# Performance work log

Hardware: AMD Instinct MI355X
Metric: run time of the kernel (lower is better)

The kernel has to match this reference:

```python
import jax, jax.numpy as jnp
import numpy as np
from jax import lax

D_MODEL = 1024
D_FF = 4096
K = 5
PAD = K // 2


def setup_inputs() -> dict:
    key = jax.random.key(0)
    ks = jax.random.split(key, 12)
    s_in = 1.0 / np.sqrt(D_MODEL)
    s_ff = 1.0 / np.sqrt(D_FF)
    s_k = 1.0 / np.sqrt(K)  # depthwise conv fan_in = 1*K
    return {
        "x": jax.random.normal(ks[0], (4, 2048, D_MODEL), dtype=jnp.float32),
        "Wg": jax.random.uniform(ks[1], (D_MODEL, D_FF), jnp.float32, -s_in, s_in),
        "bg": jax.random.uniform(ks[2], (D_FF,), jnp.float32, -s_in, s_in),
        "Wu": jax.random.uniform(ks[3], (D_MODEL, D_FF), jnp.float32, -s_in, s_in),
        "bu": jax.random.uniform(ks[4], (D_FF,), jnp.float32, -s_in, s_in),
        "convg_w": jax.random.uniform(ks[5], (D_FF, 1, K), jnp.float32, -s_k, s_k),
        "convg_b": jax.random.uniform(ks[6], (D_FF,), jnp.float32, -s_k, s_k),
        "convu_w": jax.random.uniform(ks[7], (D_FF, 1, K), jnp.float32, -s_k, s_k),
        "convu_b": jax.random.uniform(ks[8], (D_FF,), jnp.float32, -s_k, s_k),
        "Wd": jax.random.uniform(ks[9], (D_FF, D_MODEL), jnp.float32, -s_ff, s_ff),
        "bd": jax.random.uniform(ks[10], (D_MODEL,), jnp.float32, -s_ff, s_ff),
    }


def _dwconv(h, w, b):
    # h: [B, L, C] -> depthwise conv along L with 'same' padding -> [B, L, C]
    y = lax.conv_general_dilated(
        h.transpose(0, 2, 1),  # [B, C, L]
        w,                      # [C, 1, K]
        window_strides=(1,),
        padding=[(PAD, PAD)],
        feature_group_count=h.shape[-1],
    )
    return (y + b[None, :, None]).transpose(0, 2, 1)


def reference(x, Wg, bg, Wu, bu, convg_w, convg_b, convu_w, convu_b, Wd, bd):
    gate = _dwconv(jnp.einsum("bld,df->blf", x, Wg) + bg, convg_w, convg_b)
    up = _dwconv(jnp.einsum("bld,df->blf", x, Wu) + bu, convu_w, convu_b)
    h = jax.nn.silu(gate) * up
    return jnp.einsum("blf,fd->bld", h, Wd) + bd
```

## Files before the change

### kernel.cpp

```cpp
#include <hip/hip_runtime.h>
#include <hip/hip_bf16.h>
#include <cstdint>

#define BATCH  4
#define SEQ    2048
#define DMODEL 1024
#define DFF    4096
#define MTOT   (BATCH * SEQ)
#define KCONV  5
#define PADC   2

using bf16raw = unsigned short;
typedef __attribute__((ext_vector_type(8))) short bf16x8;
typedef __attribute__((ext_vector_type(4))) float f32x4;

__device__ __forceinline__ float bf2f(bf16raw u) {
    return __uint_as_float(((uint32_t)u) << 16);
}
__device__ __forceinline__ bf16raw f2bf(float f) {
    uint32_t u = __float_as_uint(f);
    u = (u + 0x7fffu + ((u >> 16) & 1u)) >> 16;
    return (bf16raw)u;
}


__global__ __launch_bounds__(256)
void cvt_bf16_kernel(const float* __restrict__ in, bf16raw* __restrict__ out, int n4)
{
    const int i = blockIdx.x * 256 + threadIdx.x;
    if (i >= n4) return;
    const float4 v = reinterpret_cast<const float4*>(in)[i];
    ushort4 o;
    o.x = f2bf(v.x); o.y = f2bf(v.y); o.z = f2bf(v.z); o.w = f2bf(v.w);
    reinterpret_cast<ushort4*>(out)[i] = o;
}

__global__ __launch_bounds__(256)
void transpose_cvt_kernel(const float* __restrict__ in, bf16raw* __restrict__ out,
                          int R, int C)
{
    __shared__ float tile[32][33];
    const int r0 = blockIdx.y * 32, c0 = blockIdx.x * 32;
    const int tx = threadIdx.x & 31, ty = threadIdx.x >> 5;
#pragma unroll
    for (int i = 0; i < 4; ++i)
        tile[ty + i * 8][tx] = in[(size_t)(r0 + ty + i * 8) * C + c0 + tx];
    __syncthreads();
#pragma unroll
    for (int i = 0; i < 4; ++i)
        out[(size_t)(c0 + ty + i * 8) * R + r0 + tx] = f2bf(tile[tx][ty + i * 8]);
}

__global__ __launch_bounds__(256)
void convw_reorder_kernel(const float* __restrict__ wg, const float* __restrict__ wu,
                          float* __restrict__ wgT, float* __restrict__ wuT)
{
    const int i = blockIdx.x * 256 + threadIdx.x;
    if (i >= KCONV * DFF) return;
    const int j = i / DFF, f = i - j * DFF;
    wgT[i] = wg[f * KCONV + j];
    wuT[i] = wu[f * KCONV + j];
}


__device__ __forceinline__ void async_load16(const bf16raw* g, bf16raw* lds)
{
    __builtin_amdgcn_global_load_lds(
        (const __attribute__((address_space(1))) void*)g,
        (__attribute__((address_space(3))) void*)lds, 16, 0, 0);
}

template<typename CT>
__global__ __launch_bounds__(256)
void mfma_gemm_kernel(const bf16raw* __restrict__ A, const bf16raw* __restrict__ BT,
                      const float* __restrict__ bias, CT* __restrict__ C,
                      int N, int K)
{
    __shared__ __align__(16) bf16raw smem[2 * 128 * 64];
    bf16raw* As = smem;
    bf16raw* Bs = smem + 128 * 64;

    const int tid  = threadIdx.x;
    const int lane = tid & 63;
    const int wave = __builtin_amdgcn_readfirstlane(tid >> 6);
    const int bm = blockIdx.y * 128;
    const int bn = blockIdx.x * 128;
    const int wm = (wave >> 1) * 64;
    const int wn = (wave & 1) * 64;

    const int srow = (wave << 3) + (lane >> 3);
    const int scol = (lane & 7) << 3;
    const bf16raw* Ag = A  + (size_t)(bm + srow) * K + scol;
    const bf16raw* Bg = BT + (size_t)(bn + srow) * K + scol;

    f32x4 acc[4][4];
#pragma unroll
    for (int i = 0; i < 4; ++i)
#pragma unroll
        for (int j = 0; j < 4; ++j) acc[i][j] = (f32x4){0.f, 0.f, 0.f, 0.f};

    for (int k0 = 0; k0 < K; k0 += 64) {
        __syncthreads();
#pragma unroll
        for (int r = 0; r < 4; ++r) {
            async_load16(Ag + (size_t)(r * 32) * K + k0, As + r * 2048 + wave * 512);
            async_load16(Bg + (size_t)(r * 32) * K + k0, Bs + r * 2048 + wave * 512);
        }
        asm volatile("s_waitcnt vmcnt(0)" ::: "memory");
        __syncthreads();

#pragma unroll
        for (int kk = 0; kk < 2; ++kk) {
            const int kb = kk * 32 + ((lane >> 4) << 3);
            bf16x8 a[4], b[4];
#pragma unroll
            for (int i = 0; i < 4; ++i) {
                a[i] = *reinterpret_cast<const bf16x8*>(As + (wm + i * 16 + (lane & 15)) * 64 + kb);
                b[i] = *reinterpret_cast<const bf16x8*>(Bs + (wn + i * 16 + (lane & 15)) * 64 + kb);
            }
#pragma unroll
            for (int mi = 0; mi < 4; ++mi)
#pragma unroll
                for (int ni = 0; ni < 4; ++ni)
                    acc[mi][ni] = __builtin_amdgcn_mfma_f32_16x16x32_bf16(
                        a[mi], b[ni], acc[mi][ni], 0, 0, 0);
        }
    }

    const int crow0 = (lane >> 4) << 2;
    const int ccol  = lane & 15;
#pragma unroll
    for (int ni = 0; ni < 4; ++ni) {
        const int n = bn + wn + ni * 16 + ccol;
        const float bs = bias[n];
#pragma unroll
        for (int mi = 0; mi < 4; ++mi) {
            const int mbase = bm + wm + mi * 16 + crow0;
#pragma unroll
            for (int j = 0; j < 4; ++j) {
                const float v = acc[mi][ni][j] + bs;
                if constexpr (sizeof(CT) == 2)
                    C[(size_t)(mbase + j) * N + n] = f2bf(v);
                else
                    C[(size_t)(mbase + j) * N + n] = v;
            }
        }
    }
}

__global__ __launch_bounds__(256)
void conv_silu_mul_bf16_kernel(const bf16raw* __restrict__ gp, const bf16raw* __restrict__ up,
                               const float* __restrict__ wgT, const float* __restrict__ cbg,
                               const float* __restrict__ wuT, const float* __restrict__ cbu,
                               bf16raw* __restrict__ h, int rows)
{
    const int idx = blockIdx.x * 256 + threadIdx.x;
    const int f   = (idx & (DFF / 8 - 1)) << 3;
    const int row = idx >> 9;
    if (row >= rows) return;
    const int l = row & (SEQ - 1);

    float g[8], u[8];
    {
        const float4 a0 = *reinterpret_cast<const float4*>(cbg + f);
        const float4 a1 = *reinterpret_cast<const float4*>(cbg + f + 4);
        const float4 b0 = *reinterpret_cast<const float4*>(cbu + f);
        const float4 b1 = *reinterpret_cast<const float4*>(cbu + f + 4);
        g[0]=a0.x; g[1]=a0.y; g[2]=a0.z; g[3]=a0.w; g[4]=a1.x; g[5]=a1.y; g[6]=a1.z; g[7]=a1.w;
        u[0]=b0.x; u[1]=b0.y; u[2]=b0.z; u[3]=b0.w; u[4]=b1.x; u[5]=b1.y; u[6]=b1.z; u[7]=b1.w;
    }

#pragma unroll
    for (int j = 0; j < KCONV; ++j) {
        const int ls = l + j - PADC;
        if (ls < 0 || ls >= SEQ) continue;
        const size_t off = (size_t)(row + j - PADC) * DFF + f;
        const bf16x8 gv = *reinterpret_cast<const bf16x8*>(gp + off);
        const bf16x8 uv = *reinterpret_cast<const bf16x8*>(up + off);
        const float4 wa0 = *reinterpret_cast<const float4*>(wgT + j * DFF + f);
        const float4 wa1 = *reinterpret_cast<const float4*>(wgT + j * DFF + f + 4);
        const float4 wb0 = *reinterpret_cast<const float4*>(wuT + j * DFF + f);
        const float4 wb1 = *reinterpret_cast<const float4*>(wuT + j * DFF + f + 4);
        const float wg8[8] = {wa0.x, wa0.y, wa0.z, wa0.w, wa1.x, wa1.y, wa1.z, wa1.w};
        const float wu8[8] = {wb0.x, wb0.y, wb0.z, wb0.w, wb1.x, wb1.y, wb1.z, wb1.w};
#pragma unroll
        for (int c = 0; c < 8; ++c) {
            g[c] += bf2f((bf16raw)gv[c]) * wg8[c];
            u[c] += bf2f((bf16raw)uv[c]) * wu8[c];
        }
    }

    bf16x8 hv;
#pragma unroll
    for (int c = 0; c < 8; ++c) {
        const float s = g[c] / (1.f + __expf(-g[c]));
        hv[c] = (short)f2bf(s * u[c]);
    }
    *reinterpret_cast<bf16x8*>(h + (size_t)row * DFF + f) = hv;
}


#define BM 128
#define BN 128
#define BK 8

__device__ __forceinline__ void load4(const float* p, float v[4]) {
    const float4 t = *reinterpret_cast<const float4*>(p);
    v[0] = t.x; v[1] = t.y; v[2] = t.z; v[3] = t.w;
}
__device__ __forceinline__ void load4(const bf16raw* p, float v[4]) {
    const ushort4 t = *reinterpret_cast<const ushort4*>(p);
    v[0] = bf2f(t.x); v[1] = bf2f(t.y); v[2] = bf2f(t.z); v[3] = bf2f(t.w);
}
__device__ __forceinline__ void store4(float* p, const float v[4]) {
    float4 t; t.x = v[0]; t.y = v[1]; t.z = v[2]; t.w = v[3];
    *reinterpret_cast<float4*>(p) = t;
}
__device__ __forceinline__ void store4(bf16raw* p, const float v[4]) {
    ushort4 t; t.x = f2bf(v[0]); t.y = f2bf(v[1]); t.z = f2bf(v[2]); t.w = f2bf(v[3]);
    *reinterpret_cast<ushort4*>(p) = t;
}

template<typename AT, typename CT>
__global__ __launch_bounds__(256)
void sgemm_bias_kernel(const AT* __restrict__ A, const float* __restrict__ B,
                       const float* __restrict__ bias, CT* __restrict__ C,
                       int N, int K)
{
    __shared__ float As[BK][BM];
    __shared__ float Bs[BK][BN];

    const int tid = threadIdx.x;
    const int bm  = blockIdx.y * BM;
    const int bn  = blockIdx.x * BN;
    const int tx  = tid & 15;
    const int ty  = tid >> 4;

    const int arow = tid >> 1;
    const int acol = (tid & 1) * 4;
    const int brow = tid >> 5;
    const int bcol = (tid & 31) * 4;

    const AT*    Ap = A + (size_t)(bm + arow) * K + acol;
    const float* Bp = B + (size_t)brow * N + bn + bcol;

    float acc[8][8];
#pragma unroll
    for (int i = 0; i < 8; ++i)
#pragma unroll
        for (int j = 0; j < 8; ++j) acc[i][j] = 0.f;

    for (int k0 = 0; k0 < K; k0 += BK) {
        float av[4];
        load4(Ap + k0, av);
        const float4 bv = *reinterpret_cast<const float4*>(Bp + (size_t)k0 * N);

        __syncthreads();
#pragma unroll
        for (int i = 0; i < 4; ++i) As[acol + i][arow] = av[i];
        *reinterpret_cast<float4*>(&Bs[brow][bcol]) = bv;
        __syncthreads();

#pragma unroll
        for (int kk = 0; kk < BK; ++kk) {
            const float4 a0 = *reinterpret_cast<const float4*>(&As[kk][ty * 4]);
            const float4 a1 = *reinterpret_cast<const float4*>(&As[kk][64 + ty * 4]);
            const float4 b0 = *reinterpret_cast<const float4*>(&Bs[kk][tx * 4]);
            const float4 b1 = *reinterpret_cast<const float4*>(&Bs[kk][64 + tx * 4]);
            const float am[8] = {a0.x, a0.y, a0.z, a0.w, a1.x, a1.y, a1.z, a1.w};
            const float bb[8] = {b0.x, b0.y, b0.z, b0.w, b1.x, b1.y, b1.z, b1.w};
#pragma unroll
            for (int mi = 0; mi < 8; ++mi)
#pragma unroll
                for (int nj = 0; nj < 8; ++nj)
                    acc[mi][nj] += am[mi] * bb[nj];
        }
    }

#pragma unroll
    for (int mi = 0; mi < 8; ++mi) {
        const int m = bm + ((mi < 4) ? (ty * 4 + mi) : (64 + ty * 4 + (mi - 4)));
#pragma unroll
        for (int g = 0; g < 2; ++g) {
            const int n = bn + g * 64 + tx * 4;
            float o[4];
#pragma unroll
            for (int c = 0; c < 4; ++c) o[c] = acc[mi][g * 4 + c] + bias[n + c];
            store4(&C[(size_t)m * N + n], o);
        }
    }
}

template<typename PT, typename HT>
__global__ __launch_bounds__(256)
void conv_silu_mul_kernel(const PT* __restrict__ gp, const PT* __restrict__ up,
                          const float* __restrict__ wg, const float* __restrict__ cbg,
                          const float* __restrict__ wu, const float* __restrict__ cbu,
                          HT* __restrict__ hout)
{
    const int idx = blockIdx.x * 256 + threadIdx.x;
    const int f   = (idx & (DFF / 4 - 1)) * 4;
    const int l   = idx >> 10;

    float g[4], u[4];
    load4(cbg + f, g);
    load4(cbu + f, u);

#pragma unroll
    for (int j = 0; j < KCONV; ++j) {
        const int ls = l + j - PADC;
        if (ls < 0 || ls >= SEQ) continue;
        const size_t off = (size_t)ls * DFF + f;
        float gv[4], uv[4];
        load4(gp + off, gv);
        load4(up + off, uv);
#pragma unroll
        for (int c = 0; c < 4; ++c) {
            g[c] += gv[c] * wg[(f + c) * KCONV + j];
            u[c] += uv[c] * wu[(f + c) * KCONV + j];
        }
    }

    float h[4];
#pragma unroll
    for (int c = 0; c < 4; ++c) {
        const float s = g[c] / (1.f + __expf(-g[c]));
        h[c] = s * u[c];
    }
    store4(hout + (size_t)l * DFF + f, h);
}


extern "C" void kernel_launch(void* const* d_in, const int* in_sizes, int n_in,
                              void* d_out, int out_size, void* d_ws, size_t ws_size,
                              hipStream_t stream)
{
    const float* x   = (const float*)d_in[0];
    const float* Wg  = (const float*)d_in[1];
    const float* bg  = (const float*)d_in[2];
    const float* Wu  = (const float*)d_in[3];
    const float* bu  = (const float*)d_in[4];
    const float* cgw = (const float*)d_in[5];
    const float* cgb = (const float*)d_in[6];
    const float* cuw = (const float*)d_in[7];
    const float* cub = (const float*)d_in[8];
    const float* Wd  = (const float*)d_in[9];
    const float* bd  = (const float*)d_in[10];
    float* out = (float*)d_out;

    const dim3 blk(256);

    const size_t SZ_XB  = (size_t)MTOT * DMODEL * 2;
    const size_t SZ_W   = (size_t)DFF * DMODEL * 2;
    const size_t SZ_CW  = (size_t)KCONV * DFF * 4;
    const size_t SZ_PF  = (size_t)MTOT * DFF * 2;
    const size_t SZ_PB  = (size_t)SEQ  * DFF * 2;

    auto align256 = [](size_t v) { return (v + 255) & ~(size_t)255; };

    size_t cur = 0;
    const size_t oXB  = cur; cur = align256(cur + SZ_XB);
    const size_t oWgT = cur; cur = align256(cur + SZ_W);
    const size_t oWuT = cur; cur = align256(cur + SZ_W);
    const size_t oWdT = cur; cur = align256(cur + SZ_W);
    const size_t oCWg = cur; cur = align256(cur + SZ_CW);
    const size_t oCWu = cur; cur = align256(cur + SZ_CW);
    const size_t oH   = cur; cur = align256(cur + SZ_PF);
    const size_t oPRE = cur;
    const size_t needT1 = oPRE + 2 * align256(SZ_PF);
    const size_t needT2 = oPRE + 2 * align256(SZ_PB);

    if (ws_size >= needT2) {
        bf16raw* xb  = (bf16raw*)((char*)d_ws + oXB);
        bf16raw* WgT = (bf16raw*)((char*)d_ws + oWgT);
        bf16raw* WuT = (bf16raw*)((char*)d_ws + oWuT);
        bf16raw* WdT = (bf16raw*)((char*)d_ws + oWdT);
        float*   cwg = (float*)((char*)d_ws + oCWg);
        float*   cwu = (float*)((char*)d_ws + oCWu);
        bf16raw* h   = (bf16raw*)((char*)d_ws + oH);

        cvt_bf16_kernel<<<(MTOT * DMODEL / 4 + 255) / 256, blk, 0, stream>>>(x, xb, MTOT * DMODEL / 4);
        transpose_cvt_kernel<<<dim3(DFF / 32, DMODEL / 32), blk, 0, stream>>>(Wg, WgT, DMODEL, DFF);
        transpose_cvt_kernel<<<dim3(DFF / 32, DMODEL / 32), blk, 0, stream>>>(Wu, WuT, DMODEL, DFF);
        transpose_cvt_kernel<<<dim3(DMODEL / 32, DFF / 32), blk, 0, stream>>>(Wd, WdT, DFF, DMODEL);
        convw_reorder_kernel<<<(KCONV * DFF + 255) / 256, blk, 0, stream>>>(cgw, cuw, cwg, cwu);

        if (ws_size >= needT1) {
            bf16raw* gpre = (bf16raw*)((char*)d_ws + oPRE);
            bf16raw* upre = (bf16raw*)((char*)d_ws + oPRE + align256(SZ_PF));
            dim3 gu(DFF / 128, MTOT / 128);
            mfma_gemm_kernel<bf16raw><<<gu, blk, 0, stream>>>(xb, WgT, bg, gpre, DFF, DMODEL);
            mfma_gemm_kernel<bf16raw><<<gu, blk, 0, stream>>>(xb, WuT, bu, upre, DFF, DMODEL);
            const int nconv = MTOT * (DFF / 8) / 256;
            conv_silu_mul_bf16_kernel<<<nconv, blk, 0, stream>>>(gpre, upre, cwg, cgb, cwu, cub, h, MTOT);
        } else {
            bf16raw* gpre = (bf16raw*)((char*)d_ws + oPRE);
            bf16raw* upre = (bf16raw*)((char*)d_ws + oPRE + align256(SZ_PB));
            dim3 gu(DFF / 128, SEQ / 128);
            const int nconv = SEQ * (DFF / 8) / 256;
            for (int b = 0; b < BATCH; ++b) {
                const bf16raw* xbb = xb + (size_t)b * SEQ * DMODEL;
                mfma_gemm_kernel<bf16raw><<<gu, blk, 0, stream>>>(xbb, WgT, bg, gpre, DFF, DMODEL);
                mfma_gemm_kernel<bf16raw><<<gu, blk, 0, stream>>>(xbb, WuT, bu, upre, DFF, DMODEL);
                conv_silu_mul_bf16_kernel<<<nconv, blk, 0, stream>>>(
                    gpre, upre, cwg, cgb, cwu, cub, h + (size_t)b * SEQ * DFF, SEQ);
            }
        }
        dim3 gd(DMODEL / 128, MTOT / 128);
        mfma_gemm_kernel<float><<<gd, blk, 0, stream>>>(h, WdT, bd, out, DMODEL, DFF);
        return;
    }

    const size_t CE  = (size_t)SEQ * DFF;
    const size_t P32 = CE * sizeof(float);
    const size_t P16 = CE * sizeof(bf16raw);

    dim3 gu(DFF / BN, SEQ / BM);
    dim3 gdc(DMODEL / BN, SEQ / BM);
    const int nconv = SEQ * (DFF / 4) / 256;

    if (ws_size >= 3 * P32) {
        float* gpre = (float*)d_ws;
        float* upre = gpre + CE;
        float* hbuf = upre + CE;
        for (int b = 0; b < BATCH; ++b) {
            const float* xbp = x + (size_t)b * SEQ * DMODEL;
            float* outb = out + (size_t)b * SEQ * DMODEL;
            sgemm_bias_kernel<float, float><<<gu, blk, 0, stream>>>(xbp, Wg, bg, gpre, DFF, DMODEL);
            sgemm_bias_kernel<float, float><<<gu, blk, 0, stream>>>(xbp, Wu, bu, upre, DFF, DMODEL);
            conv_silu_mul_kernel<float, float><<<nconv * 2, blk, 0, stream>>>(
                gpre, upre, cgw, cgb, cuw, cub, hbuf);
            sgemm_bias_kernel<float, float><<<gdc, blk, 0, stream>>>(hbuf, Wd, bd, outb, DMODEL, DFF);
        }
    } else if (ws_size >= 3 * P16) {
        bf16raw* gpre = (bf16raw*)d_ws;
        bf16raw* upre = gpre + CE;
        bf16raw* hbuf = upre + CE;
        for (int b = 0; b < BATCH; ++b) {
            const float* xbp = x + (size_t)b * SEQ * DMODEL;
            float* outb = out + (size_t)b * SEQ * DMODEL;
            sgemm_bias_kernel<float, bf16raw><<<gu, blk, 0, stream>>>(xbp, Wg, bg, gpre, DFF, DMODEL);
            sgemm_bias_kernel<float, bf16raw><<<gu, blk, 0, stream>>>(xbp, Wu, bu, upre, DFF, DMODEL);
            conv_silu_mul_kernel<bf16raw, bf16raw><<<nconv * 2, blk, 0, stream>>>(
                gpre, upre, cgw, cgb, cuw, cub, hbuf);
            sgemm_bias_kernel<bf16raw, float><<<gdc, blk, 0, stream>>>(hbuf, Wd, bd, outb, DMODEL, DFF);
        }
    }
}
```

Measured before the change: 441.5 us.

## Use 256x256 double-buffered MFMA GEMM with fused gate/up and split-K down projection

Result: faster. 386.2 us (-12.5%).

```diff
diff --git a/kernel.cpp b/kernel.cpp
--- a/kernel.cpp
+++ b/kernel.cpp
@@ -63,102 +63,165 @@
 }
 
 
-__device__ __forceinline__ void async_load16(const bf16raw* g, bf16raw* lds)
+__device__ __forceinline__ void gll16(const bf16raw* g, const char* lds)
 {
     __builtin_amdgcn_global_load_lds(
         (const __attribute__((address_space(1))) void*)g,
         (__attribute__((address_space(3))) void*)lds, 16, 0, 0);
 }
 
-template<typename CT>
-__global__ __launch_bounds__(256)
-void mfma_gemm_kernel(const bf16raw* __restrict__ A, const bf16raw* __restrict__ BT,
-                      const float* __restrict__ bias, CT* __restrict__ C,
-                      int N, int K)
-{
-    __shared__ __align__(16) bf16raw smem[2 * 128 * 64];
-    bf16raw* As = smem;
-    bf16raw* Bs = smem + 128 * 64;
+template<typename CT, bool BIAS, int SPLITK>
+__global__ __launch_bounds__(512, 2)
+void gemm256_kernel(const bf16raw* __restrict__ A, const bf16raw* __restrict__ BT,
+                    const float* __restrict__ bias0, const float* __restrict__ bias1,
+                    CT* __restrict__ C, int M, int N, int K, int nbm, int nbn)
+{
+    __shared__ __align__(16) char smem[131072];
 
     const int tid  = threadIdx.x;
     const int lane = tid & 63;
     const int wave = __builtin_amdgcn_readfirstlane(tid >> 6);
-    const int bm = blockIdx.y * 128;
-    const int bn = blockIdx.x * 128;
-    const int wm = (wave >> 1) * 64;
-    const int wn = (wave & 1) * 64;
-
-    const int srow = (wave << 3) + (lane >> 3);
-    const int scol = (lane & 7) << 3;
-    const bf16raw* Ag = A  + (size_t)(bm + srow) * K + scol;
-    const bf16raw* Bg = BT + (size_t)(bn + srow) * K + scol;
-
-    f32x4 acc[4][4];
-#pragma unroll
-    for (int i = 0; i < 4; ++i)
+    const int wr = wave >> 2;
+    const int wc = wave & 3;
+
+    const int nwg = nbm * nbn * SPLITK;
+    const int cpx = nwg >> 3;
+    const int bid = blockIdx.x;
+    const int swz = (bid & 7) * cpx + (bid >> 3);
+    int sk = 0, rem = swz;
+    if constexpr (SPLITK > 1) { sk = swz / (nbm * nbn); rem = swz - sk * (nbm * nbn); }
+    const int bx = rem / nbm;
+    const int by = rem - bx * nbm;
+    const int bm = by * 256;
+    const int bn = bx * 256;
+
+    const int klen = K / SPLITK;
+    const int kbeg = sk * klen;
+    const int NT   = klen / 64;
+    CT* Cp = C + (size_t)sk * M * N;
+
+    const int srow = tid >> 3;
+    const int kswz = (((tid & 7) ^ ((tid >> 3) & 7)) << 3);
+    const bf16raw* Asrc = A  + (size_t)(bm + srow) * K + kbeg + kswz;
+    const bf16raw* Bsrc = BT + (size_t)(bn + srow) * K + kbeg + kswz;
+
+    const int g4  = lane >> 4;
+    const int r15 = lane & 15;
+    const int key = lane & 7;
+    const int off0 = r15 * 128 + (((0 + g4) ^ key) << 4);
+    const int off1 = r15 * 128 + (((4 + g4) ^ key) << 4);
+
+    f32x4 acc[8][4];
+#pragma unroll
+    for (int i = 0; i < 8; ++i)
 #pragma unroll
         for (int j = 0; j < 4; ++j) acc[i][j] = (f32x4){0.f, 0.f, 0.f, 0.f};
 
-    for (int k0 = 0; k0 < K; k0 += 64) {
-        __syncthreads();
-#pragma unroll
-        for (int r = 0; r < 4; ++r) {
-            async_load16(Ag + (size_t)(r * 32) * K + k0, As + r * 2048 + wave * 512);
-            async_load16(Bg + (size_t)(r * 32) * K + k0, Bs + r * 2048 + wave * 512);
-        }
-        asm volatile("s_waitcnt vmcnt(0)" ::: "memory");
-        __syncthreads();
-
-#pragma unroll
-        for (int kk = 0; kk < 2; ++kk) {
-            const int kb = kk * 32 + ((lane >> 4) << 3);
-            bf16x8 a[4], b[4];
-#pragma unroll
-            for (int i = 0; i < 4; ++i) {
-                a[i] = *reinterpret_cast<const bf16x8*>(As + (wm + i * 16 + (lane & 15)) * 64 + kb);
-                b[i] = *reinterpret_cast<const bf16x8*>(Bs + (wn + i * 16 + (lane & 15)) * 64 + kb);
+    auto stage = [&](int t, int buf) {
+        const bf16raw* Ag = Asrc + (size_t)t * 64;
+        const bf16raw* Bg = Bsrc + (size_t)t * 64;
+        const char* la = smem + buf * 65536 + tid * 16;
+        const char* lb = la + 32768;
+#pragma unroll
+        for (int i = 0; i < 4; ++i) {
+            gll16(Ag + (size_t)i * 64 * K, la + i * 8192);
+            gll16(Bg + (size_t)i * 64 * K, lb + i * 8192);
+        }
+    };
+
+    auto compute = [&](int buf) {
+        const char* bufA = smem + buf * 65536 + wr * 16384;
+        const char* bufB = smem + buf * 65536 + 32768 + wc * 8192;
+        bf16x8 bfr[4][2];
+#pragma unroll
+        for (int nf = 0; nf < 4; ++nf) {
+            bfr[nf][0] = *(const bf16x8*)(bufB + nf * 2048 + off0);
+            bfr[nf][1] = *(const bf16x8*)(bufB + nf * 2048 + off1);
+        }
+#pragma unroll
+        for (int q = 0; q < 4; ++q) {
+            bf16x8 afr[2][2];
+#pragma unroll
+            for (int m2 = 0; m2 < 2; ++m2) {
+                afr[m2][0] = *(const bf16x8*)(bufA + (q * 2 + m2) * 2048 + off0);
+                afr[m2][1] = *(const bf16x8*)(bufA + (q * 2 + m2) * 2048 + off1);
             }
-#pragma unroll
-            for (int mi = 0; mi < 4; ++mi)
-#pragma unroll
-                for (int ni = 0; ni < 4; ++ni)
-                    acc[mi][ni] = __builtin_amdgcn_mfma_f32_16x16x32_bf16(
-                        a[mi], b[ni], acc[mi][ni], 0, 0, 0);
-        }
-    }
-
-    const int crow0 = (lane >> 4) << 2;
-    const int ccol  = lane & 15;
-#pragma unroll
-    for (int ni = 0; ni < 4; ++ni) {
-        const int n = bn + wn + ni * 16 + ccol;
-        const float bs = bias[n];
-#pragma unroll
-        for (int mi = 0; mi < 4; ++mi) {
-            const int mbase = bm + wm + mi * 16 + crow0;
+            __builtin_amdgcn_s_setprio(1);
+#pragma unroll
+            for (int m2 = 0; m2 < 2; ++m2)
+#pragma unroll
+                for (int nf = 0; nf < 4; ++nf) {
+                    acc[q * 2 + m2][nf] = __builtin_amdgcn_mfma_f32_16x16x32_bf16(
+                        afr[m2][0], bfr[nf][0], acc[q * 2 + m2][nf], 0, 0, 0);
+                    acc[q * 2 + m2][nf] = __builtin_amdgcn_mfma_f32_16x16x32_bf16(
+                        afr[m2][1], bfr[nf][1], acc[q * 2 + m2][nf], 0, 0, 0);
+                }
+            __builtin_amdgcn_s_setprio(0);
+        }
+    };
+
+    stage(0, 0);
+    for (int t = 0; t < NT; ++t) {
+        const int cur = t & 1;
+        if (t + 1 < NT) {
+            stage(t + 1, cur ^ 1);
+            asm volatile("s_waitcnt vmcnt(8)" ::: "memory");
+        } else {
+            asm volatile("s_waitcnt vmcnt(0)" ::: "memory");
+        }
+        __builtin_amdgcn_s_barrier();
+        compute(cur);
+        __builtin_amdgcn_s_barrier();
+        asm volatile("" ::: "memory");
+    }
+
+    const int er = g4 << 2;
+#pragma unroll
+    for (int nf = 0; nf < 4; ++nf) {
+        const int nn = bn + wc * 64 + nf * 16 + r15;
+        float bv = 0.f;
+        if constexpr (BIAS) bv = (nn < DFF) ? bias0[nn] : bias1[nn - DFF];
+#pragma unroll
+        for (int mf = 0; mf < 8; ++mf) {
+            const int mrow = bm + wr * 128 + mf * 16 + er;
 #pragma unroll
             for (int j = 0; j < 4; ++j) {
-                const float v = acc[mi][ni][j] + bs;
+                const float v = acc[mf][nf][j] + bv;
                 if constexpr (sizeof(CT) == 2)
-                    C[(size_t)(mbase + j) * N + n] = f2bf(v);
+                    Cp[(size_t)(mrow + j) * N + nn] = f2bf(v);
                 else
-                    C[(size_t)(mbase + j) * N + n] = v;
+                    Cp[(size_t)(mrow + j) * N + nn] = v;
             }
         }
     }
+}
+
+__global__ __launch_bounds__(256)
+void reduce_bias_kernel(const float* __restrict__ part, const float* __restrict__ bd,
+                        float* __restrict__ out)
+{
+    const int i = blockIdx.x * 256 + threadIdx.x;
+    const int d = (i & (DMODEL / 4 - 1)) * 4;
+    const float4 a = reinterpret_cast<const float4*>(part)[i];
+    const float4 b = reinterpret_cast<const float4*>(part + (size_t)MTOT * DMODEL)[i];
+    const float4 bb = *reinterpret_cast<const float4*>(bd + d);
+    float4 o;
+    o.x = a.x + b.x + bb.x; o.y = a.y + b.y + bb.y;
+    o.z = a.z + b.z + bb.z; o.w = a.w + b.w + bb.w;
+    reinterpret_cast<float4*>(out)[i] = o;
 }
 
 __global__ __launch_bounds__(256)
 void conv_silu_mul_bf16_kernel(const bf16raw* __restrict__ gp, const bf16raw* __restrict__ up,
                                const float* __restrict__ wgT, const float* __restrict__ cbg,
                                const float* __restrict__ wuT, const float* __restrict__ cbu,
-                               bf16raw* __restrict__ h, int rows)
+                               bf16raw* __restrict__ h, int S)
 {
     const int idx = blockIdx.x * 256 + threadIdx.x;
     const int f   = (idx & (DFF / 8 - 1)) << 3;
     const int row = idx >> 9;
-    if (row >= rows) return;
-    const int l = row & (SEQ - 1);
+    const int l   = row & (SEQ - 1);
+    const int rb  = row - l;
 
     float g[8], u[8];
     {
@@ -174,7 +237,7 @@
     for (int j = 0; j < KCONV; ++j) {
         const int ls = l + j - PADC;
         if (ls < 0 || ls >= SEQ) continue;
-        const size_t off = (size_t)(row + j - PADC) * DFF + f;
+        const size_t off = (size_t)(rb + ls) * S + f;
         const bf16x8 gv = *reinterpret_cast<const bf16x8*>(gp + off);
         const bf16x8 uv = *reinterpret_cast<const bf16x8*>(up + off);
         const float4 wa0 = *reinterpret_cast<const float4*>(wgT + j * DFF + f);
@@ -204,27 +267,14 @@
 #define BN 128
 #define BK 8
 
-__device__ __forceinline__ void load4(const float* p, float v[4]) {
+__device__ __forceinline__ void load4f(const float* p, float v[4]) {
     const float4 t = *reinterpret_cast<const float4*>(p);
     v[0] = t.x; v[1] = t.y; v[2] = t.z; v[3] = t.w;
 }
-__device__ __forceinline__ void load4(const bf16raw* p, float v[4]) {
-    const ushort4 t = *reinterpret_cast<const ushort4*>(p);
-    v[0] = bf2f(t.x); v[1] = bf2f(t.y); v[2] = bf2f(t.z); v[3] = bf2f(t.w);
-}
-__device__ __forceinline__ void store4(float* p, const float v[4]) {
-    float4 t; t.x = v[0]; t.y = v[1]; t.z = v[2]; t.w = v[3];
-    *reinterpret_cast<float4*>(p) = t;
-}
-__device__ __forceinline__ void store4(bf16raw* p, const float v[4]) {
-    ushort4 t; t.x = f2bf(v[0]); t.y = f2bf(v[1]); t.z = f2bf(v[2]); t.w = f2bf(v[3]);
-    *reinterpret_cast<ushort4*>(p) = t;
-}
-
-template<typename AT, typename CT>
-__global__ __launch_bounds__(256)
-void sgemm_bias_kernel(const AT* __restrict__ A, const float* __restrict__ B,
-                       const float* __restrict__ bias, CT* __restrict__ C,
+
+__global__ __launch_bounds__(256)
+void sgemm_bias_kernel(const float* __restrict__ A, const float* __restrict__ B,
+                       const float* __restrict__ bias, float* __restrict__ C,
                        int N, int K)
 {
     __shared__ float As[BK][BM];
@@ -241,7 +291,7 @@
     const int brow = tid >> 5;
     const int bcol = (tid & 31) * 4;
 
-    const AT*    Ap = A + (size_t)(bm + arow) * K + acol;
+    const float* Ap = A + (size_t)(bm + arow) * K + acol;
     const float* Bp = B + (size_t)brow * N + bn + bcol;
 
     float acc[8][8];
@@ -252,15 +302,13 @@
 
     for (int k0 = 0; k0 < K; k0 += BK) {
         float av[4];
-        load4(Ap + k0, av);
+        load4f(Ap + k0, av);
         const float4 bv = *reinterpret_cast<const float4*>(Bp + (size_t)k0 * N);
-
         __syncthreads();
 #pragma unroll
         for (int i = 0; i < 4; ++i) As[acol + i][arow] = av[i];
         *reinterpret_cast<float4*>(&Bs[brow][bcol]) = bv;
         __syncthreads();
-
 #pragma unroll
         for (int kk = 0; kk < BK; ++kk) {
             const float4 a0 = *reinterpret_cast<const float4*>(&As[kk][ty * 4]);
@@ -276,58 +324,57 @@
                     acc[mi][nj] += am[mi] * bb[nj];
         }
     }
-
 #pragma unroll
     for (int mi = 0; mi < 8; ++mi) {
         const int m = bm + ((mi < 4) ? (ty * 4 + mi) : (64 + ty * 4 + (mi - 4)));
 #pragma unroll
         for (int g = 0; g < 2; ++g) {
             const int n = bn + g * 64 + tx * 4;
-            float o[4];
-#pragma unroll
-            for (int c = 0; c < 4; ++c) o[c] = acc[mi][g * 4 + c] + bias[n + c];
-            store4(&C[(size_t)m * N + n], o);
-        }
-    }
-}
-
-template<typename PT, typename HT>
-__global__ __launch_bounds__(256)
-void conv_silu_mul_kernel(const PT* __restrict__ gp, const PT* __restrict__ up,
-                          const float* __restrict__ wg, const float* __restrict__ cbg,
-                          const float* __restrict__ wu, const float* __restrict__ cbu,
-                          HT* __restrict__ hout)
+            float4 o;
+            o.x = acc[mi][g * 4 + 0] + bias[n + 0];
+            o.y = acc[mi][g * 4 + 1] + bias[n + 1];
+            o.z = acc[mi][g * 4 + 2] + bias[n + 2];
+            o.w = acc[mi][g * 4 + 3] + bias[n + 3];
+            *reinterpret_cast<float4*>(&C[(size_t)m * N + n]) = o;
+        }
+    }
+}
+
+__global__ __launch_bounds__(256)
+void conv_silu_mul_f32_kernel(const float* __restrict__ gp, const float* __restrict__ up,
+                              const float* __restrict__ wg, const float* __restrict__ cbg,
+                              const float* __restrict__ wu, const float* __restrict__ cbu,
+                              float* __restrict__ hout)
 {
     const int idx = blockIdx.x * 256 + threadIdx.x;
     const int f   = (idx & (DFF / 4 - 1)) * 4;
     const int l   = idx >> 10;
 
     float g[4], u[4];
-    load4(cbg + f, g);
-    load4(cbu + f, u);
-
+    load4f(cbg + f, g);
+    load4f(cbu + f, u);
 #pragma unroll
     for (int j = 0; j < KCONV; ++j) {
         const int ls = l + j - PADC;
         if (ls < 0 || ls >= SEQ) continue;
         const size_t off = (size_t)ls * DFF + f;
         float gv[4], uv[4];
-        load4(gp + off, gv);
-        load4(up + off, uv);
+        load4f(gp + off, gv);
+        load4f(up + off, uv);
 #pragma unroll
         for (int c = 0; c < 4; ++c) {
             g[c] += gv[c] * wg[(f + c) * KCONV + j];
             u[c] += uv[c] * wu[(f + c) * KCONV + j];
         }
     }
-
     float h[4];
 #pragma unroll
     for (int c = 0; c < 4; ++c) {
         const float s = g[c] / (1.f + __expf(-g[c]));
         h[c] = s * u[c];
     }
-    store4(hout + (size_t)l * DFF + f, h);
+    float4 o; o.x = h[0]; o.y = h[1]; o.z = h[2]; o.w = h[3];
+    *reinterpret_cast<float4*>(&hout[(size_t)l * DFF + f]) = o;
 }
 
 
@@ -349,101 +396,75 @@
     float* out = (float*)d_out;
 
     const dim3 blk(256);
+    auto align256 = [](size_t v) { return (v + 255) & ~(size_t)255; };
 
     const size_t SZ_XB  = (size_t)MTOT * DMODEL * 2;
-    const size_t SZ_W   = (size_t)DFF * DMODEL * 2;
+    const size_t SZ_WGU = (size_t)2 * DFF * DMODEL * 2;
+    const size_t SZ_WD  = (size_t)DMODEL * DFF * 2;
     const size_t SZ_CW  = (size_t)KCONV * DFF * 4;
-    const size_t SZ_PF  = (size_t)MTOT * DFF * 2;
-    const size_t SZ_PB  = (size_t)SEQ  * DFF * 2;
-
-    auto align256 = [](size_t v) { return (v + 255) & ~(size_t)255; };
+    const size_t SZ_H   = (size_t)MTOT * DFF * 2;
+    const size_t SZ_UP  = (size_t)MTOT * 2 * DFF * 2;
 
     size_t cur = 0;
     const size_t oXB  = cur; cur = align256(cur + SZ_XB);
-    const size_t oWgT = cur; cur = align256(cur + SZ_W);
-    const size_t oWuT = cur; cur = align256(cur + SZ_W);
-    const size_t oWdT = cur; cur = align256(cur + SZ_W);
+    const size_t oWGU = cur; cur = align256(cur + SZ_WGU);
+    const size_t oWD  = cur; cur = align256(cur + SZ_WD);
     const size_t oCWg = cur; cur = align256(cur + SZ_CW);
     const size_t oCWu = cur; cur = align256(cur + SZ_CW);
-    const size_t oH   = cur; cur = align256(cur + SZ_PF);
-    const size_t oPRE = cur;
-    const size_t needT1 = oPRE + 2 * align256(SZ_PF);
-    const size_t needT2 = oPRE + 2 * align256(SZ_PB);
-
-    if (ws_size >= needT2) {
-        bf16raw* xb  = (bf16raw*)((char*)d_ws + oXB);
-        bf16raw* WgT = (bf16raw*)((char*)d_ws + oWgT);
-        bf16raw* WuT = (bf16raw*)((char*)d_ws + oWuT);
-        bf16raw* WdT = (bf16raw*)((char*)d_ws + oWdT);
-        float*   cwg = (float*)((char*)d_ws + oCWg);
-        float*   cwu = (float*)((char*)d_ws + oCWu);
-        bf16raw* h   = (bf16raw*)((char*)d_ws + oH);
+    const size_t oH   = cur; cur = align256(cur + SZ_H);
+    const size_t oUP  = cur; cur = align256(cur + SZ_UP);
+    const size_t need = cur;
+
+    if (ws_size >= need) {
+        bf16raw* xb   = (bf16raw*)((char*)d_ws + oXB);
+        bf16raw* Wgu  = (bf16raw*)((char*)d_ws + oWGU);
+        bf16raw* WdT  = (bf16raw*)((char*)d_ws + oWD);
+        float*   cwg  = (float*)((char*)d_ws + oCWg);
+        float*   cwu  = (float*)((char*)d_ws + oCWu);
+        bf16raw* h    = (bf16raw*)((char*)d_ws + oH);
+        bf16raw* Cup  = (bf16raw*)((char*)d_ws + oUP);
+        float*   part = (float*)((char*)d_ws + oUP);
 
         cvt_bf16_kernel<<<(MTOT * DMODEL / 4 + 255) / 256, blk, 0, stream>>>(x, xb, MTOT * DMODEL / 4);
-        transpose_cvt_kernel<<<dim3(DFF / 32, DMODEL / 32), blk, 0, stream>>>(Wg, WgT, DMODEL, DFF);
-        transpose_cvt_kernel<<<dim3(DFF / 32, DMODEL / 32), blk, 0, stream>>>(Wu, WuT, DMODEL, DFF);
+        transpose_cvt_kernel<<<dim3(DFF / 32, DMODEL / 32), blk, 0, stream>>>(Wg, Wgu, DMODEL, DFF);
+        transpose_cvt_kernel<<<dim3(DFF / 32, DMODEL / 32), blk, 0, stream>>>(Wu, Wgu + (size_t)DFF * DMODEL, DMODEL, DFF);
         transpose_cvt_kernel<<<dim3(DMODEL / 32, DFF / 32), blk, 0, stream>>>(Wd, WdT, DFF, DMODEL);
         convw_reorder_kernel<<<(KCONV * DFF + 255) / 256, blk, 0, stream>>>(cgw, cuw, cwg, cwu);
 
-        if (ws_size >= needT1) {
-            bf16raw* gpre = (bf16raw*)((char*)d_ws + oPRE);
-            bf16raw* upre = (bf16raw*)((char*)d_ws + oPRE + align256(SZ_PF));
-            dim3 gu(DFF / 128, MTOT / 128);
-            mfma_gemm_kernel<bf16raw><<<gu, blk, 0, stream>>>(xb, WgT, bg, gpre, DFF, DMODEL);
-            mfma_gemm_kernel<bf16raw><<<gu, blk, 0, stream>>>(xb, WuT, bu, upre, DFF, DMODEL);
-            const int nconv = MTOT * (DFF / 8) / 256;
-            conv_silu_mul_bf16_kernel<<<nconv, blk, 0, stream>>>(gpre, upre, cwg, cgb, cwu, cub, h, MTOT);
-        } else {
-            bf16raw* gpre = (bf16raw*)((char*)d_ws + oPRE);
-            bf16raw* upre = (bf16raw*)((char*)d_ws + oPRE + align256(SZ_PB));
-            dim3 gu(DFF / 128, SEQ / 128);
-            const int nconv = SEQ * (DFF / 8) / 256;
-            for (int b = 0; b < BATCH; ++b) {
-                const bf16raw* xbb = xb + (size_t)b * SEQ * DMODEL;
-                mfma_gemm_kernel<bf16raw><<<gu, blk, 0, stream>>>(xbb, WgT, bg, gpre, DFF, DMODEL);
-                mfma_gemm_kernel<bf16raw><<<gu, blk, 0, stream>>>(xbb, WuT, bu, upre, DFF, DMODEL);
-                conv_silu_mul_bf16_kernel<<<nconv, blk, 0, stream>>>(
-                    gpre, upre, cwg, cgb, cwu, cub, h + (size_t)b * SEQ * DFF, SEQ);
-            }
-        }
-        dim3 gd(DMODEL / 128, MTOT / 128);
-        mfma_gemm_kernel<float><<<gd, blk, 0, stream>>>(h, WdT, bd, out, DMODEL, DFF);
+        {
+            const int nbm = MTOT / 256, nbn = (2 * DFF) / 256;
+            gemm256_kernel<bf16raw, true, 1><<<nbm * nbn, dim3(512), 0, stream>>>(
+                xb, Wgu, bg, bu, Cup, MTOT, 2 * DFF, DMODEL, nbm, nbn);
+        }
+
+        conv_silu_mul_bf16_kernel<<<MTOT * (DFF / 8) / 256, blk, 0, stream>>>(
+            Cup, Cup + DFF, cwg, cgb, cwu, cub, h, 2 * DFF);
+
+        {
+            const int nbm = MTOT / 256, nbn = DMODEL / 256;
+            gemm256_kernel<float, false, 2><<<nbm * nbn * 2, dim3(512), 0, stream>>>(
+                h, WdT, nullptr, nullptr, part, MTOT, DMODEL, DFF, nbm, nbn);
+        }
+        reduce_bias_kernel<<<MTOT * DMODEL / 4 / 256, blk, 0, stream>>>(part, bd, out);
         return;
     }
 
     const size_t CE  = (size_t)SEQ * DFF;
     const size_t P32 = CE * sizeof(float);
-    const size_t P16 = CE * sizeof(bf16raw);
-
+    if (ws_size < 3 * P32) return;
+
+    float* gpre = (float*)d_ws;
+    float* upre = gpre + CE;
+    float* hbuf = upre + CE;
     dim3 gu(DFF / BN, SEQ / BM);
     dim3 gdc(DMODEL / BN, SEQ / BM);
     const int nconv = SEQ * (DFF / 4) / 256;
-
-    if (ws_size >= 3 * P32) {
-        float* gpre = (float*)d_ws;
-        float* upre = gpre + CE;
-        float* hbuf = upre + CE;
-        for (int b = 0; b < BATCH; ++b) {
-            const float* xbp = x + (size_t)b * SEQ * DMODEL;
-            float* outb = out + (size_t)b * SEQ * DMODEL;
-            sgemm_bias_kernel<float, float><<<gu, blk, 0, stream>>>(xbp, Wg, bg, gpre, DFF, DMODEL);
-            sgemm_bias_kernel<float, float><<<gu, blk, 0, stream>>>(xbp, Wu, bu, upre, DFF, DMODEL);
-            conv_silu_mul_kernel<float, float><<<nconv * 2, blk, 0, stream>>>(
-                gpre, upre, cgw, cgb, cuw, cub, hbuf);
-            sgemm_bias_kernel<float, float><<<gdc, blk, 0, stream>>>(hbuf, Wd, bd, outb, DMODEL, DFF);
-        }
-    } else if (ws_size >= 3 * P16) {
-        bf16raw* gpre = (bf16raw*)d_ws;
-        bf16raw* upre = gpre + CE;
-        bf16raw* hbuf = upre + CE;
-        for (int b = 0; b < BATCH; ++b) {
-            const float* xbp = x + (size_t)b * SEQ * DMODEL;
-            float* outb = out + (size_t)b * SEQ * DMODEL;
-            sgemm_bias_kernel<float, bf16raw><<<gu, blk, 0, stream>>>(xbp, Wg, bg, gpre, DFF, DMODEL);
-            sgemm_bias_kernel<float, bf16raw><<<gu, blk, 0, stream>>>(xbp, Wu, bu, upre, DFF, DMODEL);
-            conv_silu_mul_kernel<bf16raw, bf16raw><<<nconv * 2, blk, 0, stream>>>(
-                gpre, upre, cgw, cgb, cuw, cub, hbuf);
-            sgemm_bias_kernel<bf16raw, float><<<gdc, blk, 0, stream>>>(hbuf, Wd, bd, outb, DMODEL, DFF);
-        }
-    }
-}
+    for (int b = 0; b < BATCH; ++b) {
+        const float* xbp = x + (size_t)b * SEQ * DMODEL;
+        float* outb = out + (size_t)b * SEQ * DMODEL;
+        sgemm_bias_kernel<<<gu, blk, 0, stream>>>(xbp, Wg, bg, gpre, DFF, DMODEL);
+        sgemm_bias_kernel<<<gu, blk, 0, stream>>>(xbp, Wu, bu, upre, DFF, DMODEL);
+        conv_silu_mul_f32_kernel<<<nconv, blk, 0, stream>>>(gpre, upre, cgw, cgb, cuw, cub, hbuf);
+        sgemm_bias_kernel<<<gdc, blk, 0, stream>>>(hbuf, Wd, bd, outb, DMODEL, DFF);
+    }
+}
```
